# Kernel tuning notes

Hardware: AMD Instinct MI355X
Metric: run time of the kernel (lower is better)

The kernel has to match this reference:

```python
import jax, jax.numpy as jnp
import numpy as np
import math

B, T, A, Z, E, H = 4, 16, 512, 512, 64, 8
HD = Z // H
NF = 6  # num Fourier freqs


def setup_inputs() -> dict:
    key = jax.random.key(0)
    ks = jax.random.split(key, 16)
    w = lambda k, shape: jax.random.normal(k, shape, jnp.float32) * 0.02
    return dict(
        z_current=jax.random.normal(ks[0], (B, A, Z), jnp.float32),
        z_pred=jax.random.normal(ks[1], (B, T, A, Z), jnp.float32),
        actions=jax.random.normal(ks[2], (B, T, 4), jnp.float32),
        Wq=w(ks[3], (Z, Z)), Wk=w(ks[4], (Z, Z)), Wv=w(ks[5], (Z, Z)),
        We=w(ks[6], (E, Z)), Wo=w(ks[7], (Z, Z)),
        g_lnq=jnp.ones((Z,), jnp.float32), b_lnq=jnp.zeros((Z,), jnp.float32),
        g_lno=jnp.ones((Z,), jnp.float32), b_lno=jnp.zeros((Z,), jnp.float32),
        W_ff1=w(ks[8], (Z, 4 * Z)), b_ff1=jnp.zeros((4 * Z,), jnp.float32),
        W_ff2=w(ks[9], (4 * Z, Z)), b_ff2=jnp.zeros((Z,), jnp.float32),
        W_edge=w(ks[10], (3 * 2 * NF + 2, E)), b_edge=jnp.zeros((E,), jnp.float32),
        Wg1=w(ks[11], (2 * Z, Z)), bg1=jnp.zeros((Z,), jnp.float32),
        Wg2=w(ks[12], (Z, 1)), bg2=jnp.zeros((1,), jnp.float32),
    )


def _ln(x, g, b, eps=1e-5):
    m = jnp.mean(x, -1, keepdims=True)
    v = jnp.var(x, -1, keepdims=True)
    return (x - m) * jax.lax.rsqrt(v + eps) * g + b


def _fourier(a3):
    # a3: [B,T,3] -> [B,T, 2 + 6*NF]
    dx, dy, th = a3[..., 0:1], a3[..., 1:2], a3[..., 2:3]
    feats = [jnp.sin(th), jnp.cos(th)]
    for k in range(NF):
        f = (2.0 ** k) * math.pi
        feats += [jnp.sin(f * dx), jnp.cos(f * dx),
                  jnp.sin(f * dy), jnp.cos(f * dy),
                  jnp.sin(f * th), jnp.cos(f * th)]
    return jnp.concatenate(feats, -1)


def reference(z_current, z_pred, actions, Wq, Wk, Wv, We, Wo,
              g_lnq, b_lnq, g_lno, b_lno, W_ff1, b_ff1, W_ff2, b_ff2,
              W_edge, b_edge, Wg1, bg1, Wg2, bg2):
    q = _ln(z_pred, g_lnq, b_lnq) @ Wq                      # [B,T,A,Z]
    kc = z_current @ Wk                                      # [B,A,Z]
    vc = z_current @ Wv                                      # [B,A,Z]
    e = (_fourier(actions[..., :3]) @ W_edge + b_edge) @ We  # [B,T,Z]
    k = kc[:, None, :, :] + e[:, :, None, :]                 # [B,T,A,Z] (edge-biased keys)

    qh = q.reshape(B, T, A, H, HD)
    kh = k.reshape(B, T, A, H, HD)
    vh = vc.reshape(B, A, H, HD)

    # Non-standard attention: outer product over head INDEX (i,j in [0,H)),
    # elementwise along head_dim d -> logits [B,T,A,HD,H,H]
    logits = jnp.einsum('btaid,btajd->btadij', qh, kh) / math.sqrt(HD)
    attn = jax.lax.stop_gradient(jax.nn.softmax(logits, axis=-1))  # torch @no_grad softmax
    out_h = jnp.einsum('btadij,bajd->btaid', attn, vh)       # [B,T,A,H,HD]
    out = out_h.reshape(B, T, A, Z) @ Wo

    gate_inp = jnp.concatenate([out, z_pred], -1)            # [B,T,A,2Z]
    g = jax.nn.sigmoid(
        jax.nn.gelu(gate_inp @ Wg1 + bg1, approximate=False) @ Wg2 + bg2)  # [B,T,A,1]

    z_mid = _ln(z_pred + g * out, g_lno, b_lno)
    return z_mid + (jax.nn.gelu(z_mid @ W_ff1 + b_ff1, approximate=False) @ W_ff2 + b_ff2)
```

## Files before the change

### kernel.cpp

```cpp
#include <hip/hip_runtime.h>
#include <hip/hip_bf16.h>
#include <math.h>


typedef __bf16 bf16x8 __attribute__((ext_vector_type(8)));
typedef __bf16 bf16x4 __attribute__((ext_vector_type(4)));
typedef float f32x4 __attribute__((ext_vector_type(4)));

#define ROWS 32768
#define ZDIM 512

__device__ __forceinline__ void gload16(const void* gptr, void* ldsptr) {
  __builtin_amdgcn_global_load_lds(
      (const __attribute__((address_space(1))) unsigned int*)gptr,
      (__attribute__((address_space(3))) unsigned int*)ldsptr, 16, 0, 0);
}

__device__ __forceinline__ float gelu_f(float x) {
  return 0.5f * x * (1.0f + erff(x * 0.70710678118654752f));
}

__global__ void transpose_f32_bf16(const float* __restrict__ in,
                                   __bf16* __restrict__ out, int R, int C) {
  __shared__ float tile[32][33];
  int c0 = blockIdx.x * 32, r0 = blockIdx.y * 32;
#pragma unroll
  for (int i = 0; i < 32; i += 8)
    tile[i + threadIdx.y][threadIdx.x] =
        in[(size_t)(r0 + i + threadIdx.y) * C + c0 + threadIdx.x];
  __syncthreads();
#pragma unroll
  for (int i = 0; i < 32; i += 8)
    out[(size_t)(c0 + i + threadIdx.y) * R + r0 + threadIdx.x] =
        (__bf16)tile[threadIdx.x][i + threadIdx.y];
}

__global__ void cvt_f32_bf16(const float* __restrict__ in,
                             __bf16* __restrict__ out) {
  int i = (blockIdx.x * 256 + threadIdx.x) * 4;
  float4 v = *(const float4*)(in + i);
  out[i + 0] = (__bf16)v.x;
  out[i + 1] = (__bf16)v.y;
  out[i + 2] = (__bf16)v.z;
  out[i + 3] = (__bf16)v.w;
}

template <bool GATED, bool EMIT_RAW>
__global__ __launch_bounds__(256) void ln_kernel(
    const float* __restrict__ xa, const __bf16* __restrict__ xb,
    const float* __restrict__ gate, const float* __restrict__ gamma,
    const float* __restrict__ beta, __bf16* __restrict__ out,
    __bf16* __restrict__ raw) {
  int row = blockIdx.x;
  int tid = threadIdx.x;
  int i0 = tid * 2;
  const float* ra = xa + (size_t)row * ZDIM;
  float x0 = ra[i0], x1 = ra[i0 + 1];
  if (EMIT_RAW) {
    raw[(size_t)row * ZDIM + i0] = (__bf16)x0;
    raw[(size_t)row * ZDIM + i0 + 1] = (__bf16)x1;
  }
  if (GATED) {
    float gv = gate[row];
    const __bf16* rb = xb + (size_t)row * ZDIM;
    x0 += gv * (float)rb[i0];
    x1 += gv * (float)rb[i0 + 1];
  }
  float s = x0 + x1, s2 = x0 * x0 + x1 * x1;
#pragma unroll
  for (int off = 32; off > 0; off >>= 1) {
    s += __shfl_down(s, off);
    s2 += __shfl_down(s2, off);
  }
  __shared__ float red[8];
  int wave = tid >> 6, lane = tid & 63;
  if (lane == 0) { red[wave] = s; red[4 + wave] = s2; }
  __syncthreads();
  float ts = red[0] + red[1] + red[2] + red[3];
  float ts2 = red[4] + red[5] + red[6] + red[7];
  float mean = ts * (1.0f / ZDIM);
  float var = ts2 * (1.0f / ZDIM) - mean * mean;
  float rstd = rsqrtf(var + 1e-5f);
  float y0 = (x0 - mean) * rstd * gamma[i0] + beta[i0];
  float y1 = (x1 - mean) * rstd * gamma[i0 + 1] + beta[i0 + 1];
  out[(size_t)row * ZDIM + i0] = (__bf16)y0;
  out[(size_t)row * ZDIM + i0 + 1] = (__bf16)y1;
}

__global__ void edge_kernel(const float* __restrict__ actions,
                            const float* __restrict__ W_edge,
                            const float* __restrict__ b_edge,
                            const float* __restrict__ We,
                            float* __restrict__ e) {
  int bt = blockIdx.x;
  int tid = threadIdx.x;
  float dx = actions[bt * 4 + 0];
  float dy = actions[bt * 4 + 1];
  float th = actions[bt * 4 + 2];
  float feats[38];
  feats[0] = sinf(th);
  feats[1] = cosf(th);
  int idx = 2;
  float f = 3.14159265358979323846f;
#pragma unroll
  for (int k = 0; k < 6; k++) {
    feats[idx++] = sinf(f * dx);
    feats[idx++] = cosf(f * dx);
    feats[idx++] = sinf(f * dy);
    feats[idx++] = cosf(f * dy);
    feats[idx++] = sinf(f * th);
    feats[idx++] = cosf(f * th);
    f *= 2.0f;
  }
  __shared__ float hid[64];
  float h = b_edge[tid];
  for (int ff = 0; ff < 38; ff++) h += feats[ff] * W_edge[ff * 64 + tid];
  hid[tid] = h;
  __syncthreads();
#pragma unroll
  for (int i = 0; i < 8; i++) {
    int z = i * 64 + tid;
    float sacc = 0.0f;
    for (int j = 0; j < 64; j++) sacc += hid[j] * We[j * ZDIM + z];
    e[(size_t)bt * ZDIM + z] = sacc;
  }
}

__global__ __launch_bounds__(256) void attn_kernel(
    const __bf16* __restrict__ q, const __bf16* __restrict__ kvc,
    const float* __restrict__ e, __bf16* __restrict__ attn_out) {
  int row = blockIdx.x * 4 + (threadIdx.x >> 6);
  int lane = threadIdx.x & 63;
  int a = row & 511;
  int bt = row >> 9;
  int b = bt >> 4;
  const __bf16* qr = q + (size_t)row * ZDIM;
  const __bf16* kr = kvc + ((size_t)b * 512 + a) * 1024;
  const __bf16* vr = kr + 512;
  const float* er = e + (size_t)bt * ZDIM;
  float kv[8], vv[8], qv[8];
#pragma unroll
  for (int j = 0; j < 8; j++) {
    kv[j] = (float)kr[j * 64 + lane] + er[j * 64 + lane];
    vv[j] = (float)vr[j * 64 + lane];
  }
#pragma unroll
  for (int i = 0; i < 8; i++) qv[i] = (float)qr[i * 64 + lane];
  const float scale = 0.125f;
#pragma unroll
  for (int i = 0; i < 8; i++) {
    float lg[8], m = -1e30f;
#pragma unroll
    for (int j = 0; j < 8; j++) {
      lg[j] = qv[i] * kv[j] * scale;
      m = fmaxf(m, lg[j]);
    }
    float ssum = 0.0f, o = 0.0f;
#pragma unroll
    for (int j = 0; j < 8; j++) {
      float p = __expf(lg[j] - m);
      ssum += p;
      o += p * vv[j];
    }
    attn_out[(size_t)row * ZDIM + i * 64 + lane] = (__bf16)(o / ssum);
  }
}

__global__ __launch_bounds__(256) void gate_kernel(
    const __bf16* __restrict__ hg, const float* __restrict__ Wg2,
    const float* __restrict__ bg2, float* __restrict__ g) {
  int row = blockIdx.x * 4 + (threadIdx.x >> 6);
  int lane = threadIdx.x & 63;
  float s = 0.0f;
#pragma unroll
  for (int i = 0; i < 8; i++) {
    int z = i * 64 + lane;
    s += (float)hg[(size_t)row * ZDIM + z] * Wg2[z];
  }
#pragma unroll
  for (int off = 32; off > 0; off >>= 1) s += __shfl_down(s, off);
  if (lane == 0) g[row] = 1.0f / (1.0f + expf(-(s + bg2[0])));
}

template <bool CONCAT, int EPI, typename OT>
__global__ __launch_bounds__(256) void gemm_kernel(
    const __bf16* __restrict__ A1, const __bf16* __restrict__ A2, int ksplit,
    int lda, const __bf16* __restrict__ Bt, const float* __restrict__ bias,
    const __bf16* __restrict__ resid, OT* __restrict__ C, int N, int K) {
  __shared__ __align__(16) __bf16 As[2][128 * 32];
  __shared__ __align__(16) __bf16 Bs[2][128 * 32];
  const int tid = threadIdx.x;
  const int wave = tid >> 6, lane = tid & 63;
  const int m0 = blockIdx.x * 128, n0 = blockIdx.y * 128;
  const int scol = (lane & 3) * 8;
  const int wm = (wave & 1) * 64, wn = (wave >> 1) * 64;
  const int fr = lane & 15, fq = lane >> 4;
  const int srow = lane >> 2;

  f32x4 acc[4][4] = {};

  auto issue = [&](int kt, int buf) {
    const __bf16* Ap;
    int ka;
    if (CONCAT) {
      if (kt < ksplit) { Ap = A1; ka = kt; }
      else             { Ap = A2; ka = kt - ksplit; }
    } else { Ap = A1; ka = kt; }
#pragma unroll
    for (int c = 0; c < 2; c++) {
      int r = 32 * wave + 16 * c + srow;
      gload16(Ap + (size_t)(m0 + r) * lda + ka + scol,
              &As[buf][(32 * wave + 16 * c) * 32]);
      gload16(Bt + (size_t)(n0 + r) * K + kt + scol,
              &Bs[buf][(32 * wave + 16 * c) * 32]);
    }
  };

  const int nk = K >> 5;
  issue(0, 0);
  for (int ki = 0; ki < nk; ki++) {
    const int cur = ki & 1;
    __syncthreads();
    if (ki + 1 < nk) issue((ki + 1) << 5, cur ^ 1);
    bf16x8 af[4], bfr[4];
#pragma unroll
    for (int t = 0; t < 4; t++) {
      af[t] = *(const bf16x8*)&As[cur][(wm + t * 16 + fr) * 32 + fq * 8];
      bfr[t] = *(const bf16x8*)&Bs[cur][(wn + t * 16 + fr) * 32 + fq * 8];
    }
#pragma unroll
    for (int mt = 0; mt < 4; mt++)
#pragma unroll
      for (int nt = 0; nt < 4; nt++)
        acc[mt][nt] = __builtin_amdgcn_mfma_f32_16x16x32_bf16(
            bfr[nt], af[mt], acc[mt][nt], 0, 0, 0);
  }

#pragma unroll
  for (int mt = 0; mt < 4; mt++) {
    int m = m0 + wm + mt * 16 + fr;
#pragma unroll
    for (int nt = 0; nt < 4; nt++) {
      int nb = n0 + wn + nt * 16 + fq * 4;
      float v[4];
#pragma unroll
      for (int r = 0; r < 4; r++) v[r] = acc[mt][nt][r];
      if (EPI == 1) {
        const float4 bv = *(const float4*)&bias[nb];
#pragma unroll
        for (int r = 0; r < 4; r++)
          v[r] = gelu_f(v[r] + ((const float*)&bv)[r]);
      } else if (EPI == 2) {
        const float4 bv = *(const float4*)&bias[nb];
        const bf16x4 rv = *(const bf16x4*)&resid[(size_t)m * N + nb];
#pragma unroll
        for (int r = 0; r < 4; r++)
          v[r] += ((const float*)&bv)[r] + (float)rv[r];
      }
      if (sizeof(OT) == 2) {
        bf16x4 o;
#pragma unroll
        for (int r = 0; r < 4; r++) o[r] = (__bf16)v[r];
        *(bf16x4*)&C[(size_t)m * N + nb] = o;
      } else {
        float4 o = make_float4(v[0], v[1], v[2], v[3]);
        *(float4*)&C[(size_t)m * N + nb] = o;
      }
    }
  }
}

extern "C" void kernel_launch(void* const* d_in, const int* in_sizes, int n_in,
                              void* d_out, int out_size, void* d_ws,
                              size_t ws_size, hipStream_t stream) {
  const float* z_current = (const float*)d_in[0];
  const float* z_pred = (const float*)d_in[1];
  const float* actions = (const float*)d_in[2];
  const float* Wq = (const float*)d_in[3];
  const float* Wk = (const float*)d_in[4];
  const float* Wv = (const float*)d_in[5];
  const float* We = (const float*)d_in[6];
  const float* Wo = (const float*)d_in[7];
  const float* g_lnq = (const float*)d_in[8];
  const float* b_lnq = (const float*)d_in[9];
  const float* g_lno = (const float*)d_in[10];
  const float* b_lno = (const float*)d_in[11];
  const float* W_ff1 = (const float*)d_in[12];
  const float* b_ff1 = (const float*)d_in[13];
  const float* W_ff2 = (const float*)d_in[14];
  const float* b_ff2 = (const float*)d_in[15];
  const float* W_edge = (const float*)d_in[16];
  const float* b_edge = (const float*)d_in[17];
  const float* Wg1 = (const float*)d_in[18];
  const float* bg1 = (const float*)d_in[19];
  const float* Wg2 = (const float*)d_in[20];
  const float* bg2 = (const float*)d_in[21];

  char* ws = (char*)d_ws;
  size_t off = 0;
  auto alloc = [&](size_t bytes) {
    void* p = ws + off;
    off += (bytes + 255) & ~(size_t)255;
    return p;
  };
  __bf16* WTkv = (__bf16*)alloc(1024 * 512 * 2);
  __bf16* WTq = (__bf16*)alloc(512 * 512 * 2);
  __bf16* WTo = (__bf16*)alloc(512 * 512 * 2);
  __bf16* WTg1 = (__bf16*)alloc(512 * 1024 * 2);
  __bf16* WTf1 = (__bf16*)alloc(2048 * 512 * 2);
  __bf16* WTf2 = (__bf16*)alloc(512 * 2048 * 2);
  __bf16* zc_bf = (__bf16*)alloc(2048 * 512 * 2);
  __bf16* zp_bf = (__bf16*)alloc((size_t)ROWS * ZDIM * 2);
  __bf16* kvc = (__bf16*)alloc(2048 * 1024 * 2);
  float* ebuf = (float*)alloc(64 * 512 * 4);
  float* gbuf = (float*)alloc(32768 * 4);
  __bf16* BUF_A = (__bf16*)alloc((size_t)2 * ROWS * ZDIM * 2);
  __bf16* BUF_B = BUF_A + (size_t)ROWS * ZDIM;
  __bf16* BUF_C = (__bf16*)alloc((size_t)ROWS * ZDIM * 2);
  (void)ws_size; (void)in_sizes; (void)n_in; (void)out_size;

  dim3 tb(32, 8);
  transpose_f32_bf16<<<dim3(16, 16), tb, 0, stream>>>(Wk, WTkv, 512, 512);
  transpose_f32_bf16<<<dim3(16, 16), tb, 0, stream>>>(Wv, WTkv + 512 * 512,
                                                      512, 512);
  transpose_f32_bf16<<<dim3(16, 16), tb, 0, stream>>>(Wq, WTq, 512, 512);
  transpose_f32_bf16<<<dim3(16, 16), tb, 0, stream>>>(Wo, WTo, 512, 512);
  transpose_f32_bf16<<<dim3(16, 32), tb, 0, stream>>>(Wg1, WTg1, 1024, 512);
  transpose_f32_bf16<<<dim3(64, 16), tb, 0, stream>>>(W_ff1, WTf1, 512, 2048);
  transpose_f32_bf16<<<dim3(16, 64), tb, 0, stream>>>(W_ff2, WTf2, 2048, 512);

  cvt_f32_bf16<<<1024, 256, 0, stream>>>(z_current, zc_bf);
  ln_kernel<false, true><<<ROWS, 256, 0, stream>>>(z_pred, nullptr, nullptr,
                                                   g_lnq, b_lnq, BUF_A, zp_bf);
  edge_kernel<<<64, 64, 0, stream>>>(actions, W_edge, b_edge, We, ebuf);
  gemm_kernel<false, 0, __bf16><<<dim3(16, 8), 256, 0, stream>>>(
      zc_bf, nullptr, 0, 512, WTkv, nullptr, nullptr, kvc, 1024, 512);
  gemm_kernel<false, 0, __bf16><<<dim3(256, 4), 256, 0, stream>>>(
      BUF_A, nullptr, 0, 512, WTq, nullptr, nullptr, BUF_B, 512, 512);
  attn_kernel<<<ROWS / 4, 256, 0, stream>>>(BUF_B, kvc, ebuf, BUF_A);
  gemm_kernel<false, 0, __bf16><<<dim3(256, 4), 256, 0, stream>>>(
      BUF_A, nullptr, 0, 512, WTo, nullptr, nullptr, BUF_B, 512, 512);
  gemm_kernel<true, 1, __bf16><<<dim3(256, 4), 256, 0, stream>>>(
      BUF_B, zp_bf, 512, 512, WTg1, bg1, nullptr, BUF_C, 512, 1024);
  gate_kernel<<<ROWS / 4, 256, 0, stream>>>(BUF_C, Wg2, bg2, gbuf);
  ln_kernel<true, false><<<ROWS, 256, 0, stream>>>(z_pred, BUF_B, gbuf, g_lno,
                                                   b_lno, BUF_C, nullptr);
  float* outp = (float*)d_out;
  __bf16* h1 = BUF_A;
  for (int c = 0; c < 2; c++) {
    const __bf16* zmid_c = BUF_C + (size_t)c * 16384 * 512;
    gemm_kernel<false, 1, __bf16><<<dim3(128, 16), 256, 0, stream>>>(
        zmid_c, nullptr, 0, 512, WTf1, b_ff1, nullptr, h1, 2048, 512);
    gemm_kernel<false, 2, float><<<dim3(128, 4), 256, 0, stream>>>(
        h1, nullptr, 0, 2048, WTf2, b_ff2, zmid_c,
        outp + (size_t)c * 16384 * 512, 512, 2048);
  }
}
```

Measured before the change: 707.2 us.

## Use XOR-swizzled single-buffered 64-wide K tiles in GEMM kernel

```diff
diff --git a/kernel.cpp b/kernel.cpp
--- a/kernel.cpp
+++ b/kernel.cpp
@@ -187,19 +187,20 @@
     const __bf16* __restrict__ A1, const __bf16* __restrict__ A2, int ksplit,
     int lda, const __bf16* __restrict__ Bt, const float* __restrict__ bias,
     const __bf16* __restrict__ resid, OT* __restrict__ C, int N, int K) {
-  __shared__ __align__(16) __bf16 As[2][128 * 32];
-  __shared__ __align__(16) __bf16 Bs[2][128 * 32];
+  __shared__ __align__(16) __bf16 As[128 * 64];
+  __shared__ __align__(16) __bf16 Bs[128 * 64];
   const int tid = threadIdx.x;
   const int wave = tid >> 6, lane = tid & 63;
   const int m0 = blockIdx.x * 128, n0 = blockIdx.y * 128;
-  const int scol = (lane & 3) * 8;
+  const int srow = lane >> 3;
+  const int gcol = ((lane & 7) ^ srow) * 8;
   const int wm = (wave & 1) * 64, wn = (wave >> 1) * 64;
   const int fr = lane & 15, fq = lane >> 4;
-  const int srow = lane >> 2;
+  const int fr7 = fr & 7;
 
   f32x4 acc[4][4] = {};
 
-  auto issue = [&](int kt, int buf) {
+  for (int kt = 0; kt < K; kt += 64) {
     const __bf16* Ap;
     int ka;
     if (CONCAT) {
@@ -207,33 +208,32 @@
       else             { Ap = A2; ka = kt - ksplit; }
     } else { Ap = A1; ka = kt; }
 #pragma unroll
-    for (int c = 0; c < 2; c++) {
-      int r = 32 * wave + 16 * c + srow;
-      gload16(Ap + (size_t)(m0 + r) * lda + ka + scol,
-              &As[buf][(32 * wave + 16 * c) * 32]);
-      gload16(Bt + (size_t)(n0 + r) * K + kt + scol,
-              &Bs[buf][(32 * wave + 16 * c) * 32]);
-    }
-  };
-
-  const int nk = K >> 5;
-  issue(0, 0);
-  for (int ki = 0; ki < nk; ki++) {
-    const int cur = ki & 1;
+    for (int c = 0; c < 4; c++) {
+      int r = 32 * wave + 8 * c + srow;
+      gload16(Ap + (size_t)(m0 + r) * lda + ka + gcol,
+              &As[(32 * wave + 8 * c) * 64]);
+      gload16(Bt + (size_t)(n0 + r) * K + kt + gcol,
+              &Bs[(32 * wave + 8 * c) * 64]);
+    }
     __syncthreads();
-    if (ki + 1 < nk) issue((ki + 1) << 5, cur ^ 1);
-    bf16x8 af[4], bfr[4];
-#pragma unroll
-    for (int t = 0; t < 4; t++) {
-      af[t] = *(const bf16x8*)&As[cur][(wm + t * 16 + fr) * 32 + fq * 8];
-      bfr[t] = *(const bf16x8*)&Bs[cur][(wn + t * 16 + fr) * 32 + fq * 8];
-    }
-#pragma unroll
-    for (int mt = 0; mt < 4; mt++)
-#pragma unroll
-      for (int nt = 0; nt < 4; nt++)
-        acc[mt][nt] = __builtin_amdgcn_mfma_f32_16x16x32_bf16(
-            bfr[nt], af[mt], acc[mt][nt], 0, 0, 0);
+#pragma unroll
+    for (int s = 0; s < 2; s++) {
+      const int g = s * 4 + fq;
+      const int col = (g ^ fr7) * 8;
+      bf16x8 af[4], bfr[4];
+#pragma unroll
+      for (int t = 0; t < 4; t++) {
+        af[t] = *(const bf16x8*)&As[(wm + t * 16 + fr) * 64 + col];
+        bfr[t] = *(const bf16x8*)&Bs[(wn + t * 16 + fr) * 64 + col];
+      }
+#pragma unroll
+      for (int mt = 0; mt < 4; mt++)
+#pragma unroll
+        for (int nt = 0; nt < 4; nt++)
+          acc[mt][nt] = __builtin_amdgcn_mfma_f32_16x16x32_bf16(
+              bfr[nt], af[mt], acc[mt][nt], 0, 0, 0);
+    }
+    __syncthreads();
   }
 
 #pragma unroll
```

Result: no change. 697.7 us (-1.4%).
